# Kernel optimization log

Hardware: AMD Instinct MI355X
Metric: run time of the kernel (lower is better)

The kernel has to match this reference:

```python
import jax, jax.numpy as jnp
import numpy as np

B, CIN, H, W = 16, 256, 32, 32
COUT = 256
DK = 128       # key depth (total over heads)
DV = 128       # attentional channels (total over heads)
NH = 8
DKH = DK // NH # 16
DVH = DV // NH # 16
CCONV = COUT - DV  # channels of the plain conv branch


def setup_inputs() -> dict:
    key = jax.random.key(0)
    ks = jax.random.split(key, 7)
    x = jax.random.normal(ks[0], (B, CIN, H, W), dtype=jnp.float32)
    # 3x3 conv branch (padding=1), OIHW
    conv_w = jax.random.normal(ks[1], (CCONV, CIN, 3, 3), dtype=jnp.float32) * 0.02
    conv_b = jnp.zeros((CCONV,), dtype=jnp.float32)
    # 1x1 qkv conv, stored as [out, in]
    qkv_w = jax.random.normal(ks[2], (2 * DK + DV, CIN), dtype=jnp.float32) * 0.02
    qkv_b = jnp.zeros((2 * DK + DV,), dtype=jnp.float32)
    # 1x1 output projection for attention branch
    attn_w = jax.random.normal(ks[3], (DV, DV), dtype=jnp.float32) * 0.02
    attn_b = jnp.zeros((DV,), dtype=jnp.float32)
    return {"x": x, "conv_w": conv_w, "conv_b": conv_b,
            "qkv_w": qkv_w, "qkv_b": qkv_b,
            "attn_w": attn_w, "attn_b": attn_b}


def reference(x, conv_w, conv_b, qkv_w, qkv_b, attn_w, attn_b):
    b, _, h, w = x.shape
    hw = h * w
    # plain conv branch: 3x3, padding 1
    conv_out = jax.lax.conv_general_dilated(
        x, conv_w, window_strides=(1, 1), padding=((1, 1), (1, 1)),
        dimension_numbers=("NCHW", "OIHW", "NCHW")) + conv_b[None, :, None, None]
    # 1x1 qkv conv
    qkv = jnp.einsum("bchw,oc->bohw", x, qkv_w) + qkv_b[None, :, None, None]
    q = qkv[:, :DK].reshape(b, NH, DKH, hw) * (DKH ** -0.5)
    k = qkv[:, DK:2 * DK].reshape(b, NH, DKH, hw)
    v = qkv[:, 2 * DK:].reshape(b, NH, DVH, hw)
    # logits[b,n,p,q] = sum_c q[b,n,c,p] * k[b,n,c,q]
    logits = jnp.einsum("bncp,bncq->bnpq", q, k)
    weights = jax.nn.softmax(logits, axis=-1)
    # attn[b,n,c,p] = sum_q v[b,n,c,q] * weights[b,n,p,q]
    attn = jnp.einsum("bncq,bnpq->bncp", v, weights).reshape(b, DV, h, w)
    attn = jnp.einsum("bchw,oc->bohw", attn, attn_w) + attn_b[None, :, None, None]
    return jnp.concatenate((conv_out, attn), axis=1)
```

## Files before the change

### kernel.cpp

```cpp
#include <hip/hip_runtime.h>
#include <cstddef>

#define B_ 16
#define CIN_ 256
#define H_ 32
#define W_ 32
#define HW_ 1024
#define COUT_ 256
#define DK_ 128
#define DV_ 128
#define NH_ 8
#define DKH_ 16
#define DVH_ 16
#define CCONV_ 128
#define QKVO_ 384

typedef __attribute__((ext_vector_type(4))) _Float16 half4v;
typedef __attribute__((ext_vector_type(8))) _Float16 half8v;
typedef __attribute__((ext_vector_type(4))) float float4v;

#define QSCALE 0.36067376022224085f

__global__ __launch_bounds__(256) void xt_kernel(
    const float* __restrict__ x, _Float16* __restrict__ xF)
{
    const int pt = blockIdx.x;
    const int ct = blockIdx.y;
    const int b  = blockIdx.z;
    __shared__ float T[32][33];
    const int t = threadIdx.x;
    const int c = t & 31, r = t >> 5;
#pragma unroll
    for (int i = 0; i < 4; ++i) {
        const int ci = ct * 32 + r + i * 8;
        T[r + i * 8][c] = x[(size_t)(b * CIN_ + ci) * HW_ + pt * 32 + c];
    }
    __syncthreads();
    const int cq = (t & 7) * 4;
    const int pi = t >> 3;
    half4v h;
#pragma unroll
    for (int j = 0; j < 4; ++j) h[j] = (_Float16)T[cq + j][pi];
    const int p = pt * 32 + pi;
    *(half4v*)(xF + ((size_t)(b * 8 + ct) * HW_ + p) * 32 + cq) = h;
}

__global__ __launch_bounds__(256) void wprep_kernel(
    const float* __restrict__ conv_w, const float* __restrict__ qkv_w,
    const float* __restrict__ attn_w, _Float16* __restrict__ wC,
    _Float16* __restrict__ wF, _Float16* __restrict__ wP)
{
    const int bid = blockIdx.x;
    const int t = threadIdx.x;
    if (bid < 128) {
        const int id = bid * 256 + t;
        const int co = id >> 8, ci = id & 255;
        const float* src = conv_w + (size_t)id * 9;
#pragma unroll
        for (int j = 0; j < 9; ++j)
            wC[(((size_t)(ci >> 5) * 9 + j) * 8 + (co >> 4)) * 512 + (co & 15) * 32 + (ci & 31)]
                = (_Float16)src[j];
    } else if (bid < 224) {
        const int g = (bid - 128) * 256 + t;
        const int o = g >> 6, k0 = (g & 63) * 4;
        const float4 v = *(const float4*)(qkv_w + (size_t)o * CIN_ + k0);
        half4v h; h[0] = (_Float16)v.x; h[1] = (_Float16)v.y;
        h[2] = (_Float16)v.z; h[3] = (_Float16)v.w;
        *(half4v*)(wF + ((size_t)(k0 >> 5) * QKVO_ + o) * 32 + (k0 & 31)) = h;
    } else {
        const int g = (bid - 224) * 256 + t;
        const int o = g >> 5, k0 = (g & 31) * 4;
        const float4 v = *(const float4*)(attn_w + (size_t)o * DV_ + k0);
        half4v h; h[0] = (_Float16)v.x; h[1] = (_Float16)v.y;
        h[2] = (_Float16)v.z; h[3] = (_Float16)v.w;
        *(half4v*)(wP + ((size_t)(k0 >> 5) * DV_ + o) * 32 + (k0 & 31)) = h;
    }
}

__global__ __launch_bounds__(256) void qkv_kernel(
    const _Float16* __restrict__ xF, const _Float16* __restrict__ wF,
    const float* __restrict__ qkv_b, _Float16* __restrict__ Qt,
    _Float16* __restrict__ Kt, _Float16* __restrict__ vF)
{
    const int pt = blockIdx.x;
    const int ot = blockIdx.y;
    const int b  = blockIdx.z;
    const int lane = threadIdx.x & 63, w = threadIdx.x >> 6;
    const int l16 = lane & 15, hi = lane >> 4;
    const int p0 = pt * 64;
    const int og = ot * 4 + w;
    const int o0 = og * 16;

    float4v acc[4];
#pragma unroll
    for (int pg = 0; pg < 4; ++pg) acc[pg] = (float4v){0.f, 0.f, 0.f, 0.f};

    for (int kc = 0; kc < 8; ++kc) {
        const half8v a = *(const half8v*)(wF + ((size_t)kc * QKVO_ + o0 + l16) * 32 + hi * 8);
#pragma unroll
        for (int pg = 0; pg < 4; ++pg) {
            const half8v bf = *(const half8v*)(xF + ((size_t)(b * 8 + kc) * HW_ + p0 + pg * 16 + l16) * 32 + hi * 8);
            acc[pg] = __builtin_amdgcn_mfma_f32_16x16x32_f16(a, bf, acc[pg], 0, 0, 0);
        }
    }

    float bias[4];
#pragma unroll
    for (int r = 0; r < 4; ++r) bias[r] = qkv_b[o0 + hi * 4 + r];

    if (og < 16) {
        const float scale = (og < 8) ? QSCALE : 1.0f;
        const int n = og & 7;
        _Float16* dst = (og < 8 ? Qt : Kt) + (size_t)(b * NH_ + n) * (HW_ * 16) + hi * 4;
#pragma unroll
        for (int pg = 0; pg < 4; ++pg) {
            const int p = p0 + pg * 16 + l16;
            half4v h;
#pragma unroll
            for (int r = 0; r < 4; ++r) h[r] = (_Float16)((acc[pg][r] + bias[r]) * scale);
            *(half4v*)(dst + (size_t)p * 16) = h;
        }
    } else {
        const int n = og - 16;
        _Float16* Vb = vF + (size_t)(b * NH_ + n) * (64 * 16 * 16);
#pragma unroll
        for (int pg = 0; pg < 4; ++pg) {
            const int qg = pt * 4 + pg;
#pragma unroll
            for (int r = 0; r < 4; ++r)
                Vb[(size_t)(qg * 16 + hi * 4 + r) * 16 + l16] = (_Float16)(acc[pg][r] + bias[r]);
        }
    }
}

__global__ __launch_bounds__(256) void attn_kernel(
    const _Float16* __restrict__ Qt, const _Float16* __restrict__ Kt,
    const _Float16* __restrict__ vF, _Float16* __restrict__ aF)
{
    const int bx = blockIdx.x;
    const int pc = bx & 7;
    const int n  = (bx >> 3) & 7;
    const int b  = bx >> 6;
    const int lane = threadIdx.x & 63, wave = threadIdx.x >> 6;
    const int pg = wave >> 1, qh = wave & 1;
    const int l16 = lane & 15, lg = lane >> 4;

    const int bn = b * NH_ + n;
    const _Float16* Qh = Qt + (size_t)bn * (HW_ * 16);
    const _Float16* Kh = Kt + (size_t)bn * (HW_ * 16);
    const _Float16* Vh = vF + (size_t)bn * (64 * 16 * 16);

    const int pbase = pc * 128 + pg * 64;

    half4v qf[4];
#pragma unroll
    for (int t = 0; t < 4; ++t)
        qf[t] = *(const half4v*)(Qh + (size_t)(pbase + t * 16 + l16) * 16 + lg * 4);

    float4v o[4];
    float rs[4];
#pragma unroll
    for (int t = 0; t < 4; ++t) { o[t] = (float4v){0.f, 0.f, 0.f, 0.f}; rs[t] = 0.f; }

    const float4v zero = (float4v){0.f, 0.f, 0.f, 0.f};

    const int q0beg = qh * 512;
    for (int q0 = q0beg; q0 < q0beg + 512; q0 += 16) {
        const half4v kf = *(const half4v*)(Kh + (size_t)(q0 + l16) * 16 + lg * 4);
        const half4v vf = *(const half4v*)(Vh + (size_t)((q0 >> 4) * 16 + l16) * 16 + lg * 4);
#pragma unroll
        for (int t = 0; t < 4; ++t) {
            float4v s = __builtin_amdgcn_mfma_f32_16x16x16f16(kf, qf[t], zero, 0, 0, 0);
            const float e0 = __builtin_amdgcn_exp2f(s[0]);
            const float e1 = __builtin_amdgcn_exp2f(s[1]);
            const float e2 = __builtin_amdgcn_exp2f(s[2]);
            const float e3 = __builtin_amdgcn_exp2f(s[3]);
            rs[t] += (e0 + e1) + (e2 + e3);
            half4v pf;
            pf[0] = (_Float16)e0; pf[1] = (_Float16)e1;
            pf[2] = (_Float16)e2; pf[3] = (_Float16)e3;
            o[t] = __builtin_amdgcn_mfma_f32_16x16x16f16(vf, pf, o[t], 0, 0, 0);
        }
    }

    __shared__ float Ored[2][64][16];
    __shared__ float Rred[2][64][4];
    if (qh == 1) {
#pragma unroll
        for (int t = 0; t < 4; ++t) {
#pragma unroll
            for (int rr = 0; rr < 4; ++rr) Ored[pg][lane][t * 4 + rr] = o[t][rr];
            Rred[pg][lane][t] = rs[t];
        }
    }
    __syncthreads();
    if (qh == 0) {
#pragma unroll
        for (int t = 0; t < 4; ++t) {
#pragma unroll
            for (int rr = 0; rr < 4; ++rr) o[t][rr] += Ored[pg][lane][t * 4 + rr];
            rs[t] += Rred[pg][lane][t];
        }
#pragma unroll
        for (int t = 0; t < 4; ++t) {
            float r = rs[t];
            r += __shfl_xor(r, 16);
            r += __shfl_xor(r, 32);
            const float inv = 1.0f / r;
            half4v h;
#pragma unroll
            for (int rr = 0; rr < 4; ++rr) h[rr] = (_Float16)(o[t][rr] * inv);
            *(half4v*)(aF + (((size_t)(b * 64 + (pbase >> 4) + t) * 4 + (n >> 1)) * 16 + l16) * 32
                          + (n & 1) * 16 + lg * 4) = h;
        }
    }
}

__global__ __launch_bounds__(256) void proj_kernel(
    const _Float16* __restrict__ aF, const _Float16* __restrict__ wP,
    const float* __restrict__ attn_b, float* __restrict__ out)
{
    const int pt = blockIdx.x;
    const int ot = blockIdx.y;
    const int b  = blockIdx.z;
    const int lane = threadIdx.x & 63, w = threadIdx.x >> 6;
    const int l16 = lane & 15, hi = lane >> 4;
    const int p0 = pt * 64;
    const int o0 = ot * 64 + w * 16;

    float4v acc[4];
#pragma unroll
    for (int pg = 0; pg < 4; ++pg) acc[pg] = (float4v){0.f, 0.f, 0.f, 0.f};

    for (int kc = 0; kc < 4; ++kc) {
        const half8v a = *(const half8v*)(wP + ((size_t)kc * DV_ + o0 + l16) * 32 + hi * 8);
#pragma unroll
        for (int pg = 0; pg < 4; ++pg) {
            const half8v bf = *(const half8v*)(aF + (((size_t)(b * 64 + pt * 4 + pg) * 4 + kc) * 16 + l16) * 32 + hi * 8);
            acc[pg] = __builtin_amdgcn_mfma_f32_16x16x32_f16(a, bf, acc[pg], 0, 0, 0);
        }
    }
#pragma unroll
    for (int pg = 0; pg < 4; ++pg) {
        const int p = p0 + pg * 16 + l16;
#pragma unroll
        for (int r = 0; r < 4; ++r) {
            const int o = o0 + hi * 4 + r;
            out[((size_t)(b * COUT_ + CCONV_ + o)) * HW_ + p] = acc[pg][r] + attn_b[o];
        }
    }
}

__global__ __launch_bounds__(256) void conv_kernel(
    const _Float16* __restrict__ xF, const _Float16* __restrict__ wC,
    const float* __restrict__ conv_b, float* __restrict__ out)
{
    const int r  = blockIdx.x;
    const int ch = blockIdx.y;
    const int b  = blockIdx.z;
    const int t = threadIdx.x;
    const int lane = t & 63, w = t >> 6;
    const int l16 = lane & 15, hi = lane >> 4;
    const int c16 = ch * 4 + w;

    const bool lane0bad  = (l16 == 0);
    const bool lane15bad = (l16 == 15);
    const half8v z = {0, 0, 0, 0, 0, 0, 0, 0};

    float4v acc[2];
    acc[0] = (float4v){0.f, 0.f, 0.f, 0.f};
    acc[1] = (float4v){0.f, 0.f, 0.f, 0.f};

    for (int kc = 0; kc < 8; ++kc) {
        const _Float16* xk = xF + ((size_t)(b * 8 + kc) * HW_ + r * 32) * 32 + l16 * 32 + hi * 8;
        const _Float16* ab = wC + ((size_t)(kc * 9) * 8 + c16) * 512 + l16 * 32 + hi * 8;
#pragma unroll
        for (int kh = 0; kh < 3; ++kh) {
            const int rr = r + kh - 1;
            if ((unsigned)rr >= 32u) continue;
#pragma unroll
            for (int kw = 0; kw < 3; ++kw) {
                const half8v a = *(const half8v*)(ab + (size_t)((kh * 3 + kw) * 8) * 512);
                const int sh = ((kh - 1) * 32 + (kw - 1)) * 32;
                half8v b0 = *(const half8v*)(xk + sh);
                half8v b1 = *(const half8v*)(xk + sh + 16 * 32);
                if (kw == 0) b0 = lane0bad  ? z : b0;
                if (kw == 2) b1 = lane15bad ? z : b1;
                acc[0] = __builtin_amdgcn_mfma_f32_16x16x32_f16(a, b0, acc[0], 0, 0, 0);
                acc[1] = __builtin_amdgcn_mfma_f32_16x16x32_f16(a, b1, acc[1], 0, 0, 0);
            }
        }
    }
#pragma unroll
    for (int rr = 0; rr < 4; ++rr) {
        const int co = c16 * 16 + hi * 4 + rr;
        const float bias = conv_b[co];
        float* dst = out + (size_t)(b * COUT_ + co) * HW_ + r * 32;
        dst[l16]      = acc[0][rr] + bias;
        dst[16 + l16] = acc[1][rr] + bias;
    }
}

extern "C" void kernel_launch(void* const* d_in, const int* in_sizes, int n_in,
                              void* d_out, int out_size, void* d_ws, size_t ws_size,
                              hipStream_t stream)
{
    (void)in_sizes; (void)n_in; (void)out_size; (void)ws_size;
    const float* x      = (const float*)d_in[0];
    const float* conv_w = (const float*)d_in[1];
    const float* conv_b = (const float*)d_in[2];
    const float* qkv_w  = (const float*)d_in[3];
    const float* qkv_b  = (const float*)d_in[4];
    const float* attn_w = (const float*)d_in[5];
    const float* attn_b = (const float*)d_in[6];
    float* out = (float*)d_out;

    char* ws = (char*)d_ws;
    _Float16* xF = (_Float16*)(ws + 4096);
    _Float16* wC = (_Float16*)(ws + 8392704);
    _Float16* wF = (_Float16*)(ws + 8982528);
    _Float16* wP = (_Float16*)(ws + 9179136);
    _Float16* Qt = (_Float16*)(ws + 9211904);
    _Float16* Kt = (_Float16*)(ws + 13406208);
    _Float16* vF = (_Float16*)(ws + 17600512);
    _Float16* aF = (_Float16*)(ws + 21794816);

    xt_kernel<<<dim3(32, 8, B_), dim3(256), 0, stream>>>(x, xF);
    wprep_kernel<<<dim3(240), dim3(256), 0, stream>>>(conv_w, qkv_w, attn_w, wC, wF, wP);
    qkv_kernel<<<dim3(16, 6, B_), dim3(256), 0, stream>>>(xF, wF, qkv_b, Qt, Kt, vF);
    attn_kernel<<<dim3(1024), dim3(256), 0, stream>>>(Qt, Kt, vF, aF);
    proj_kernel<<<dim3(16, 2, B_), dim3(256), 0, stream>>>(aF, wP, attn_b, out);
    conv_kernel<<<dim3(32, 2, B_), dim3(256), 0, stream>>>(xF, wC, conv_b, out);
}
```

Baseline: 186.0 us.

## Pre-pad and pre-shift input copies so the conv needs no boundary masking

The transpose kernel now writes three copies of the fp16 input: unshifted, shifted left and shifted right, each with zero halo rows above and below the image. The 3x3 conv can then load its operands without boundary branches or lane masks. The conv kernel also gives each wave two output-channel tiles, reusing every input fragment across two MFMAs, and launches half as many blocks. In exchange the transpose kernel writes three times the data and the workspace grows, while the conv grid shrinks to 512 blocks, which may reduce occupancy.

```diff
diff --git a/kernel.cpp b/kernel.cpp
--- a/kernel.cpp
+++ b/kernel.cpp
@@ -21,19 +21,21 @@
 
 #define QSCALE 0.36067376022224085f
 
+#define XFS_SZ ((size_t)16 * 8 * 34 * 1024)
+
 __global__ __launch_bounds__(256) void xt_kernel(
-    const float* __restrict__ x, _Float16* __restrict__ xF)
-{
-    const int pt = blockIdx.x;
-    const int ct = blockIdx.y;
-    const int b  = blockIdx.z;
+    const float* __restrict__ x, _Float16* __restrict__ xFs)
+{
+    const int row = blockIdx.x;
+    const int kc  = blockIdx.y;
+    const int b   = blockIdx.z;
     __shared__ float T[32][33];
     const int t = threadIdx.x;
     const int c = t & 31, r = t >> 5;
 #pragma unroll
     for (int i = 0; i < 4; ++i) {
-        const int ci = ct * 32 + r + i * 8;
-        T[r + i * 8][c] = x[(size_t)(b * CIN_ + ci) * HW_ + pt * 32 + c];
+        const int ci = kc * 32 + r + i * 8;
+        T[r + i * 8][c] = x[(size_t)(b * CIN_ + ci) * HW_ + row * 32 + c];
     }
     __syncthreads();
     const int cq = (t & 7) * 4;
@@ -41,8 +43,22 @@
     half4v h;
 #pragma unroll
     for (int j = 0; j < 4; ++j) h[j] = (_Float16)T[cq + j][pi];
-    const int p = pt * 32 + pi;
-    *(half4v*)(xF + ((size_t)(b * 8 + ct) * HW_ + p) * 32 + cq) = h;
+    const half4v z = {0, 0, 0, 0};
+    const size_t bk = ((size_t)b * 8 + kc) * 34;
+    const size_t rbase = (bk + row + 1) * 1024;
+    *(half4v*)(xFs + rbase + pi * 32 + cq) = h;
+    if (pi < 31) *(half4v*)(xFs + XFS_SZ + rbase + (pi + 1) * 32 + cq) = h;
+    else         *(half4v*)(xFs + XFS_SZ + rbase + 0 * 32 + cq) = z;
+    if (pi > 0)  *(half4v*)(xFs + 2 * XFS_SZ + rbase + (pi - 1) * 32 + cq) = h;
+    else         *(half4v*)(xFs + 2 * XFS_SZ + rbase + 31 * 32 + cq) = z;
+    if (row == 0) {
+        for (int i = t; i < 1536; i += 256) {
+            const int s = i / 512;
+            const int rm = (i / 256) & 1;
+            const int q = (i & 255) * 4;
+            *(half4v*)(xFs + (size_t)s * XFS_SZ + (bk + (rm ? 33 : 0)) * 1024 + q) = z;
+        }
+    }
 }
 
 __global__ __launch_bounds__(256) void wprep_kernel(
@@ -78,7 +94,7 @@
 }
 
 __global__ __launch_bounds__(256) void qkv_kernel(
-    const _Float16* __restrict__ xF, const _Float16* __restrict__ wF,
+    const _Float16* __restrict__ xFs, const _Float16* __restrict__ wF,
     const float* __restrict__ qkv_b, _Float16* __restrict__ Qt,
     _Float16* __restrict__ Kt, _Float16* __restrict__ vF)
 {
@@ -97,9 +113,10 @@
 
     for (int kc = 0; kc < 8; ++kc) {
         const half8v a = *(const half8v*)(wF + ((size_t)kc * QKVO_ + o0 + l16) * 32 + hi * 8);
+        const _Float16* xb = xFs + (((size_t)b * 8 + kc) * 34 + 1) * 1024;
 #pragma unroll
         for (int pg = 0; pg < 4; ++pg) {
-            const half8v bf = *(const half8v*)(xF + ((size_t)(b * 8 + kc) * HW_ + p0 + pg * 16 + l16) * 32 + hi * 8);
+            const half8v bf = *(const half8v*)(xb + (size_t)(p0 + pg * 16 + l16) * 32 + hi * 8);
             acc[pg] = __builtin_amdgcn_mfma_f32_16x16x32_f16(a, bf, acc[pg], 0, 0, 0);
         }
     }
@@ -252,53 +269,53 @@
 }
 
 __global__ __launch_bounds__(256) void conv_kernel(
-    const _Float16* __restrict__ xF, const _Float16* __restrict__ wC,
+    const _Float16* __restrict__ xFs, const _Float16* __restrict__ wC,
     const float* __restrict__ conv_b, float* __restrict__ out)
 {
-    const int r  = blockIdx.x;
-    const int ch = blockIdx.y;
-    const int b  = blockIdx.z;
+    const int r = blockIdx.x;
+    const int b = blockIdx.y;
     const int t = threadIdx.x;
     const int lane = t & 63, w = t >> 6;
     const int l16 = lane & 15, hi = lane >> 4;
-    const int c16 = ch * 4 + w;
-
-    const bool lane0bad  = (l16 == 0);
-    const bool lane15bad = (l16 == 15);
-    const half8v z = {0, 0, 0, 0, 0, 0, 0, 0};
-
-    float4v acc[2];
-    acc[0] = (float4v){0.f, 0.f, 0.f, 0.f};
-    acc[1] = (float4v){0.f, 0.f, 0.f, 0.f};
-
+
+    float4v acc[2][2];
+#pragma unroll
+    for (int i = 0; i < 2; ++i)
+#pragma unroll
+        for (int j = 0; j < 2; ++j) acc[i][j] = (float4v){0.f, 0.f, 0.f, 0.f};
+
+#pragma unroll
     for (int kc = 0; kc < 8; ++kc) {
-        const _Float16* xk = xF + ((size_t)(b * 8 + kc) * HW_ + r * 32) * 32 + l16 * 32 + hi * 8;
-        const _Float16* ab = wC + ((size_t)(kc * 9) * 8 + c16) * 512 + l16 * 32 + hi * 8;
+        const size_t xrow = (((size_t)b * 8 + kc) * 34 + r) * 1024 + l16 * 32 + hi * 8;
+        const _Float16* ab = wC + ((size_t)(kc * 9) * 8 + 2 * w) * 512 + l16 * 32 + hi * 8;
 #pragma unroll
         for (int kh = 0; kh < 3; ++kh) {
-            const int rr = r + kh - 1;
-            if ((unsigned)rr >= 32u) continue;
 #pragma unroll
             for (int kw = 0; kw < 3; ++kw) {
-                const half8v a = *(const half8v*)(ab + (size_t)((kh * 3 + kw) * 8) * 512);
-                const int sh = ((kh - 1) * 32 + (kw - 1)) * 32;
-                half8v b0 = *(const half8v*)(xk + sh);
-                half8v b1 = *(const half8v*)(xk + sh + 16 * 32);
-                if (kw == 0) b0 = lane0bad  ? z : b0;
-                if (kw == 2) b1 = lane15bad ? z : b1;
-                acc[0] = __builtin_amdgcn_mfma_f32_16x16x32_f16(a, b0, acc[0], 0, 0, 0);
-                acc[1] = __builtin_amdgcn_mfma_f32_16x16x32_f16(a, b1, acc[1], 0, 0, 0);
+                const int cp = (kw == 0) ? 1 : ((kw == 1) ? 0 : 2);
+                const _Float16* a = ab + (size_t)((kh * 3 + kw) * 8) * 512;
+                const half8v a0 = *(const half8v*)(a);
+                const half8v a1 = *(const half8v*)(a + 512);
+                const _Float16* xp = xFs + (size_t)cp * XFS_SZ + xrow + (size_t)kh * 1024;
+                const half8v b0 = *(const half8v*)(xp);
+                const half8v b1 = *(const half8v*)(xp + 16 * 32);
+                acc[0][0] = __builtin_amdgcn_mfma_f32_16x16x32_f16(a0, b0, acc[0][0], 0, 0, 0);
+                acc[0][1] = __builtin_amdgcn_mfma_f32_16x16x32_f16(a0, b1, acc[0][1], 0, 0, 0);
+                acc[1][0] = __builtin_amdgcn_mfma_f32_16x16x32_f16(a1, b0, acc[1][0], 0, 0, 0);
+                acc[1][1] = __builtin_amdgcn_mfma_f32_16x16x32_f16(a1, b1, acc[1][1], 0, 0, 0);
             }
         }
     }
 #pragma unroll
-    for (int rr = 0; rr < 4; ++rr) {
-        const int co = c16 * 16 + hi * 4 + rr;
-        const float bias = conv_b[co];
-        float* dst = out + (size_t)(b * COUT_ + co) * HW_ + r * 32;
-        dst[l16]      = acc[0][rr] + bias;
-        dst[16 + l16] = acc[1][rr] + bias;
-    }
+    for (int cg = 0; cg < 2; ++cg)
+#pragma unroll
+        for (int rr = 0; rr < 4; ++rr) {
+            const int co = (2 * w + cg) * 16 + hi * 4 + rr;
+            const float bias = conv_b[co];
+            float* dst = out + (size_t)(b * COUT_ + co) * HW_ + r * 32;
+            dst[l16]      = acc[cg][0][rr] + bias;
+            dst[16 + l16] = acc[cg][1][rr] + bias;
+        }
 }
 
 extern "C" void kernel_launch(void* const* d_in, const int* in_sizes, int n_in,
@@ -316,19 +333,19 @@
     float* out = (float*)d_out;
 
     char* ws = (char*)d_ws;
-    _Float16* xF = (_Float16*)(ws + 4096);
-    _Float16* wC = (_Float16*)(ws + 8392704);
-    _Float16* wF = (_Float16*)(ws + 8982528);
-    _Float16* wP = (_Float16*)(ws + 9179136);
-    _Float16* Qt = (_Float16*)(ws + 9211904);
-    _Float16* Kt = (_Float16*)(ws + 13406208);
-    _Float16* vF = (_Float16*)(ws + 17600512);
-    _Float16* aF = (_Float16*)(ws + 21794816);
-
-    xt_kernel<<<dim3(32, 8, B_), dim3(256), 0, stream>>>(x, xF);
+    _Float16* xFs = (_Float16*)(ws);
+    _Float16* wC  = (_Float16*)(ws + 26738688);
+    _Float16* wF  = (_Float16*)(ws + 27328512);
+    _Float16* wP  = (_Float16*)(ws + 27525120);
+    _Float16* Qt  = (_Float16*)(ws + 27557888);
+    _Float16* Kt  = (_Float16*)(ws + 31752192);
+    _Float16* vF  = (_Float16*)(ws + 35946496);
+    _Float16* aF  = (_Float16*)(ws + 40140800);
+
+    xt_kernel<<<dim3(32, 8, B_), dim3(256), 0, stream>>>(x, xFs);
     wprep_kernel<<<dim3(240), dim3(256), 0, stream>>>(conv_w, qkv_w, attn_w, wC, wF, wP);
-    qkv_kernel<<<dim3(16, 6, B_), dim3(256), 0, stream>>>(xF, wF, qkv_b, Qt, Kt, vF);
+    qkv_kernel<<<dim3(16, 6, B_), dim3(256), 0, stream>>>(xFs, wF, qkv_b, Qt, Kt, vF);
     attn_kernel<<<dim3(1024), dim3(256), 0, stream>>>(Qt, Kt, vF, aF);
     proj_kernel<<<dim3(16, 2, B_), dim3(256), 0, stream>>>(aF, wP, attn_b, out);
-    conv_kernel<<<dim3(32, 2, B_), dim3(256), 0, stream>>>(xF, wC, conv_b, out);
-}
+    conv_kernel<<<dim3(32, B_), dim3(256), 0, stream>>>(xFs, wC, conv_b, out);
+}
```

Result: faster. 173.1 us (-7.0%).
